# Performance work log

Measured on AMD Instinct MI355X. Metric: run time of the kernel, lower is better.

Reference implementation:

```python
import jax, jax.numpy as jnp
import numpy as np

N_EMBD = 1024
N_HEAD = 16
HEAD_DIM = N_EMBD // N_HEAD
B, T = 2, 2048


def setup_inputs() -> dict:
    key = jax.random.key(0)
    ks = jax.random.split(key, 9)
    s = 1.0 / np.sqrt(N_EMBD)
    return {
        "x": jax.random.normal(ks[0], (B, T, N_EMBD), dtype=jnp.float32),
        "Wq": jax.random.normal(ks[1], (N_EMBD, N_EMBD), dtype=jnp.float32) * s,
        "bq": jax.random.normal(ks[2], (N_EMBD,), dtype=jnp.float32) * s,
        "Wk": jax.random.normal(ks[3], (N_EMBD, N_EMBD), dtype=jnp.float32) * s,
        "bk": jax.random.normal(ks[4], (N_EMBD,), dtype=jnp.float32) * s,
        "Wv": jax.random.normal(ks[5], (N_EMBD, N_EMBD), dtype=jnp.float32) * s,
        "bv": jax.random.normal(ks[6], (N_EMBD,), dtype=jnp.float32) * s,
        "Wp": jax.random.normal(ks[7], (N_EMBD, N_EMBD), dtype=jnp.float32) * s,
        "bp": jax.random.normal(ks[8], (N_EMBD,), dtype=jnp.float32) * s,
    }


def reference(x, Wq, bq, Wk, bk, Wv, bv, Wp, bp):
    b, t, c = x.shape
    # torch Linear: y = x @ W.T + b
    def proj(W, bias):
        y = jnp.einsum('btc,oc->bto', x, W) + bias
        return y.reshape(b, t, N_HEAD, HEAD_DIM).transpose(0, 2, 1, 3)  # [B,H,T,D]

    q = proj(Wq, bq)
    k = proj(Wk, bk)
    v = proj(Wv, bv)

    scale = 1.0 / np.sqrt(HEAD_DIM).astype(np.float32)
    scores = jnp.einsum('bhqd,bhkd->bhqk', q, k) * scale  # [B,H,T,T]
    causal = jnp.tril(jnp.ones((t, t), dtype=bool))
    scores = jnp.where(causal[None, None], scores, jnp.float32(-jnp.inf))
    attn = jax.nn.softmax(scores, axis=-1)
    out = jnp.einsum('bhqk,bhkd->bhqd', attn, v)  # [B,H,T,D]
    out = out.transpose(0, 2, 1, 3).reshape(b, t, c)
    out = jnp.einsum('btc,oc->bto', out, Wp) + bp
    return out
```

## Files before the change

### kernel.cpp

```cpp
#include <hip/hip_runtime.h>
#include <hip/hip_bf16.h>

#define TT 2048
#define MM 4096

typedef __attribute__((ext_vector_type(8))) short bf16x8;
typedef __attribute__((ext_vector_type(4))) float f32x4;

__device__ inline short f2bf(float f){
  union { float f; unsigned u; } x; x.f = f;
  unsigned r = x.u + 0x7FFFu + ((x.u >> 16) & 1u);
  return (short)(r >> 16);
}
__device__ inline int pk2bf(float a, float b){
  __hip_bfloat162 h2 = __float22bfloat162_rn(make_float2(a, b));
  return *(int*)&h2;
}

__device__ inline void async16(const void* g, void* l){
  __builtin_amdgcn_global_load_lds((const __attribute__((address_space(1))) void*)g,
                                   (__attribute__((address_space(3))) void*)l, 16, 0, 0);
}

__global__ void cvt_all(const float* __restrict__ x,
                        const float* __restrict__ Wq, const float* __restrict__ Wk,
                        const float* __restrict__ Wv, const float* __restrict__ Wp,
                        short* __restrict__ xb, short* __restrict__ Wqb, short* __restrict__ Wkb,
                        short* __restrict__ Wvb, short* __restrict__ Wpb){
  int b = blockIdx.x;
  const float* in; short* out; int base;
  if (b < 4096)      { in = x;  out = xb;  base = b; }
  else if (b < 5120) { in = Wq; out = Wqb; base = b - 4096; }
  else if (b < 6144) { in = Wk; out = Wkb; base = b - 5120; }
  else if (b < 7168) { in = Wv; out = Wvb; base = b - 6144; }
  else               { in = Wp; out = Wpb; base = b - 7168; }
  int i = base * 256 + threadIdx.x;
  float4 v = ((const float4*)in)[i];
  short4 o;
  o.x = f2bf(v.x); o.y = f2bf(v.y); o.z = f2bf(v.z); o.w = f2bf(v.w);
  ((short4*)out)[i] = o;
}

__device__ inline void gemm_core(const short* __restrict__ A, const short* __restrict__ Wm,
                                 short* As, short* Bs, int m0, int n0, int k0, int nkt,
                                 int tid, int wm, int wn, int quad, int lr,
                                 f32x4 acc[4][4])
{
  const int prow = tid >> 2, pcol = (tid & 3) << 3;
  const short* Ap0 = A  + (size_t)(m0 + prow) * 1024 + k0 + pcol;
  const short* Ap1 = Ap0 + 64 * 1024;
  const short* Bp0 = Wm + (size_t)(n0 + prow) * 1024 + k0 + pcol;
  const short* Bp1 = Bp0 + 64 * 1024;
  for (int kt = 0; kt < nkt; ++kt){
    const int kk = kt * 64;
#pragma unroll
    for (int pn = 0; pn < 2; ++pn){
      async16(Ap0 + kk + pn*32, As + pn*4096 + (size_t)tid * 8);
      async16(Ap1 + kk + pn*32, As + pn*4096 + (size_t)(tid + 256) * 8);
      async16(Bp0 + kk + pn*32, Bs + pn*4096 + (size_t)tid * 8);
      async16(Bp1 + kk + pn*32, Bs + pn*4096 + (size_t)(tid + 256) * 8);
    }
    __syncthreads();
#pragma unroll
    for (int ks = 0; ks < 2; ++ks){
      bf16x8 aF[4], bF[4];
#pragma unroll
      for (int mt = 0; mt < 4; ++mt) aF[mt] = *(const bf16x8*)(As + ks*4096 + (wm*64 + mt*16 + lr)*32 + quad*8);
#pragma unroll
      for (int nt = 0; nt < 4; ++nt) bF[nt] = *(const bf16x8*)(Bs + ks*4096 + (wn*64 + nt*16 + lr)*32 + quad*8);
#pragma unroll
      for (int mt = 0; mt < 4; ++mt)
#pragma unroll
        for (int nt = 0; nt < 4; ++nt)
          acc[mt][nt] = __builtin_amdgcn_mfma_f32_16x16x32_bf16(aF[mt], bF[nt], acc[mt][nt], 0, 0, 0);
    }
    __syncthreads();
  }
}

__launch_bounds__(256, 3)
__global__ void gemm_qkv(const short* __restrict__ A,
                         const short* __restrict__ W0, const short* __restrict__ W1, const short* __restrict__ W2,
                         const float* __restrict__ b0, const float* __restrict__ b1, const float* __restrict__ b2,
                         short* __restrict__ Qo, short* __restrict__ Ko, short* __restrict__ Vt)
{
  __shared__ __align__(16) short smem[16384];
  short* As = smem;
  short* Bs = smem + 8192;
  const int bid = blockIdx.x + (blockIdx.y << 3) + (blockIdx.z << 8);
  const int xcd = bid & 7, slot = bid >> 3;
  const int z   = slot >> 5;
  const int rem = slot & 31;
  const int m0  = (((xcd << 2) + (rem >> 3))) * 128;
  const int n0  = (rem & 7) * 128;
  const short* Wm   = (z == 0) ? W0 : ((z == 1) ? W1 : W2);
  const float* bias = (z == 0) ? b0 : ((z == 1) ? b1 : b2);
  const int tid = threadIdx.x;
  const int lane = tid & 63, wave = tid >> 6;
  const int wm = wave >> 1, wn = wave & 1;
  const int quad = lane >> 4, lr = lane & 15;

  f32x4 acc[4][4];
#pragma unroll
  for (int i = 0; i < 4; ++i)
#pragma unroll
    for (int j = 0; j < 4; ++j)
#pragma unroll
      for (int r = 0; r < 4; ++r) acc[i][j][r] = 0.f;

  gemm_core(A, Wm, As, Bs, m0, n0, 0, 16, tid, wm, wn, quad, lr, acc);

  const float qscale = 0.125f * 1.4426950408889634f;
  const int bB = m0 >> 11, t0 = m0 & 2047;

  if (z == 2){
#pragma unroll
    for (int nh = 0; nh < 2; ++nh){
      __syncthreads();
      if (wn == nh){
#pragma unroll
        for (int nt = 0; nt < 4; ++nt){
          int n = n0 + wn*64 + nt*16 + lr;
          float bv = bias[n];
          int n_l = nt*16 + lr;
#pragma unroll
          for (int mt = 0; mt < 4; ++mt)
#pragma unroll
            for (int r = 0; r < 4; ++r){
              int m_l = wm*64 + mt*16 + quad*4 + r;
              smem[n_l*136 + m_l] = f2bf(acc[mt][nt][r] + bv);
            }
        }
      }
      __syncthreads();
#pragma unroll
      for (int i = 0; i < 4; ++i){
        int c = tid + i*256;
        int rowN = c >> 4, ch = c & 15;
        int4 v = *(const int4*)(smem + rowN*136 + ch*8);
        int n = n0 + nh*64 + rowN;
        int hH = n >> 6, d = n & 63;
        *(int4*)(Vt + ((size_t)((bB<<4) + hH)*64 + d)*2048 + t0 + ch*8) = v;
      }
    }
    return;
  }

  short* dst = (z == 0) ? Qo : Ko;
#pragma unroll
  for (int nh = 0; nh < 2; ++nh){
    __syncthreads();
    if (wn == nh){
#pragma unroll
      for (int nt = 0; nt < 4; ++nt){
        int n_l = nt*16 + lr;
        float bv = bias[n0 + nh*64 + n_l];
#pragma unroll
        for (int mt = 0; mt < 4; ++mt){
#pragma unroll
          for (int r = 0; r < 4; ++r){
            int m_l = wm*64 + mt*16 + quad*4 + r;
            float v = acc[mt][nt][r] + bv;
            if (z == 0) v *= qscale;
            smem[m_l*72 + n_l] = f2bf(v);
          }
        }
      }
    }
    __syncthreads();
    const int hH = (n0 + nh*64) >> 6;
    short* dhead = dst + (size_t)((bB<<4) + hH) * 2048 * 64;
#pragma unroll
    for (int i = 0; i < 4; ++i){
      int c = tid + i*256;
      int rowm = c >> 3, ch = (c & 7) << 3;
      int4 v = *(const int4*)(smem + rowm*72 + ch);
      *(int4*)(dhead + (size_t)(t0 + rowm)*64 + ch) = v;
    }
  }
}

__launch_bounds__(256, 2)
__global__ void gemm_proj(const short* __restrict__ A, const short* __restrict__ Wm,
                          const float* __restrict__ bias, float* __restrict__ out)
{
  __shared__ __align__(16) short As[2*4096];
  __shared__ __align__(16) short Bs[2*2048];
  const int bid = blockIdx.x + (blockIdx.y << 4);
  const int xcd = bid & 7, slot = bid >> 3;
  const int m0  = ((xcd << 2) + (slot >> 4)) * 128;
  const int n0  = (slot & 15) * 64;
  const int tid = threadIdx.x;
  const int lane = tid & 63, wave = tid >> 6;
  const int quad = lane >> 4, lr = lane & 15;

  const int prow = tid >> 2, pcol = (tid & 3) << 3;
  const short* Ap0 = A  + (size_t)(m0 + prow) * 1024 + pcol;
  const short* Ap1 = Ap0 + 64 * 1024;
  const short* Bp0 = Wm + (size_t)(n0 + prow) * 1024 + pcol;

  f32x4 acc[2][4];
#pragma unroll
  for (int i = 0; i < 2; ++i)
#pragma unroll
    for (int j = 0; j < 4; ++j)
#pragma unroll
      for (int r = 0; r < 4; ++r) acc[i][j][r] = 0.f;

  for (int kt = 0; kt < 16; ++kt){
    const int kk = kt * 64;
#pragma unroll
    for (int pn = 0; pn < 2; ++pn){
      async16(Ap0 + kk + pn*32, As + pn*4096 + (size_t)tid * 8);
      async16(Ap1 + kk + pn*32, As + pn*4096 + (size_t)(tid + 256) * 8);
      async16(Bp0 + kk + pn*32, Bs + pn*2048 + (size_t)tid * 8);
    }
    __syncthreads();
#pragma unroll
    for (int ks = 0; ks < 2; ++ks){
      bf16x8 aF[2], bF[4];
#pragma unroll
      for (int mt = 0; mt < 2; ++mt) aF[mt] = *(const bf16x8*)(As + ks*4096 + (wave*32 + mt*16 + lr)*32 + quad*8);
#pragma unroll
      for (int nt = 0; nt < 4; ++nt) bF[nt] = *(const bf16x8*)(Bs + ks*2048 + (nt*16 + lr)*32 + quad*8);
#pragma unroll
      for (int mt = 0; mt < 2; ++mt)
#pragma unroll
        for (int nt = 0; nt < 4; ++nt)
          acc[mt][nt] = __builtin_amdgcn_mfma_f32_16x16x32_bf16(aF[mt], bF[nt], acc[mt][nt], 0, 0, 0);
    }
    __syncthreads();
  }

#pragma unroll
  for (int nt = 0; nt < 4; ++nt){
    int n = n0 + nt*16 + lr;
    float bv = bias[n];
#pragma unroll
    for (int mt = 0; mt < 2; ++mt){
      int mBase = m0 + wave*32 + mt*16 + quad*4;
#pragma unroll
      for (int r = 0; r < 4; ++r){
        int m = mBase + r;
        out[(size_t)m * 1024 + n] = acc[mt][nt][r] + bv;
      }
    }
  }
}

__device__ __constant__ int slice_tbl[24] = {
  14352, 30736,     2,
  31760, 26638,  2052,
  12302, 27534,  4102,
  28687, 20491,  6152,
  29647, 19082, 16393,
  24589, 10252, 16969,
  25421, 21195,  8202,
  22540, 23308, 18442
};

__launch_bounds__(256, 3)
__global__ void attn_kernel(const short* __restrict__ Q, const short* __restrict__ K,
                            const short* __restrict__ Vt, short* __restrict__ AO,
                            float* __restrict__ Opart, float* __restrict__ Lpart)
{
  __shared__ __align__(16) short Ks[2][4096];
  __shared__ __align__(16) short Vs[2][4096];
  __shared__ __align__(16) short Ps[8192];
  const int tid = threadIdx.x, lane = tid & 63, wave = tid >> 6;
  const int quad = lane >> 4, lr = lane & 15;
  const int bid = blockIdx.x;
  const int a = (bid >> 5) & 7;
  const int hb = bid & 31;
  const int j = bid >> 8;
  const int e = slice_tbl[a*3 + j];
  const int qb = e >> 11, kv_s = (e >> 6) & 31, kvn = e & 63;
  const bool split = (kvn != 2*qb + 2);
  const int half = (kv_s != 0) ? 1 : 0;
  const int bidx = hb >> 4, h = hb & 15;
  const int wq0 = qb * 128 + wave * 32;
  const short* Qh = Q  + (size_t)hb * TT * 64;
  const short* Kh = K  + (size_t)hb * TT * 64;
  const short* Vh = Vt + (size_t)hb * 64 * TT;
  short* Pw = Ps + wave * 2048;

  const int srow = tid >> 3;
  const int ssw  = (tid & 7) ^ (srow & 7);
  const short* Kp0 = Kh + (size_t)srow * 64 + ssw * 8;
  const short* Vp0 = Vh + (size_t)srow * TT + ssw * 8;

  bf16x8 qf[2][2];
#pragma unroll
  for (int g = 0; g < 2; ++g)
#pragma unroll
    for (int ks = 0; ks < 2; ++ks)
      qf[g][ks] = *(const bf16x8*)(Qh + (size_t)(wq0 + g*16 + lr) * 64 + ks*32 + quad*8);

  const int lsw0 = (((0*4 + quad) ^ (lr & 7)) << 3);
  const int lsw1 = (((1*4 + quad) ^ (lr & 7)) << 3);
  const int qh2 = quad >> 1, qlo = (quad & 1) << 2;

  f32x4 acc_o[2][4], l_acc[2];
#pragma unroll
  for (int g = 0; g < 2; ++g){
#pragma unroll
    for (int r = 0; r < 4; ++r) l_acc[g][r] = 0.f;
#pragma unroll
    for (int dt = 0; dt < 4; ++dt)
#pragma unroll
      for (int r = 0; r < 4; ++r) acc_o[g][dt][r] = 0.f;
  }

  const short one_bf = (short)0x3F80;
  const bf16x8 onesf = { one_bf, one_bf, one_bf, one_bf, one_bf, one_bf, one_bf, one_bf };

  const int kv_e = kv_s + kvn;
  const int qtw = wq0 >> 6;
  {
    const short* kp = Kp0 + (size_t)kv_s * 4096;
    const short* vp = Vp0 + kv_s * 64;
    async16(kp,          &Ks[0][(size_t)tid * 8]);
    async16(kp + 32*64,  &Ks[0][(size_t)(tid + 256) * 8]);
    async16(vp,          &Vs[0][(size_t)tid * 8]);
    async16(vp + 32*TT,  &Vs[0][(size_t)(tid + 256) * 8]);
  }

  const short* kp_n = Kp0 + (size_t)(kv_s + 1) * 4096;
  const short* vp_n = Vp0 + (kv_s + 1) * 64;

  int cur = 0;
  for (int kv = kv_s; kv < kv_e; ++kv){
    const int kv0 = kv * 64;
    __syncthreads();
    if (kv + 1 < kv_e){
      const int nb = cur ^ 1;
      async16(kp_n,          &Ks[nb][(size_t)tid * 8]);
      async16(kp_n + 32*64,  &Ks[nb][(size_t)(tid + 256) * 8]);
      async16(vp_n,          &Vs[nb][(size_t)tid * 8]);
      async16(vp_n + 32*TT,  &Vs[nb][(size_t)(tid + 256) * 8]);
      kp_n += 4096; vp_n += 64;
    }
    if (kv0 <= wq0 + 31){
      __builtin_amdgcn_s_setprio(1);
      f32x4 s4[2][4];
#pragma unroll
      for (int g = 0; g < 2; ++g)
#pragma unroll
        for (int nt = 0; nt < 4; ++nt)
#pragma unroll
          for (int r = 0; r < 4; ++r) s4[g][nt][r] = 0.f;
#pragma unroll
      for (int nt = 0; nt < 4; ++nt){
        bf16x8 kf0 = *(const bf16x8*)(&Ks[cur][(nt*16 + lr)*64 + lsw0]);
        bf16x8 kf1 = *(const bf16x8*)(&Ks[cur][(nt*16 + lr)*64 + lsw1]);
#pragma unroll
        for (int g = 0; g < 2; ++g){
          s4[g][nt] = __builtin_amdgcn_mfma_f32_16x16x32_bf16(kf0, qf[g][0], s4[g][nt], 0, 0, 0);
          s4[g][nt] = __builtin_amdgcn_mfma_f32_16x16x32_bf16(kf1, qf[g][1], s4[g][nt], 0, 0, 0);
        }
      }

      if (kv == qtw){
#pragma unroll
        for (int g = 0; g < 2; ++g){
          const int qglob = wq0 + g*16 + lr;
          short* Pg = Pw + g*1024;
#pragma unroll
          for (int nt = 0; nt < 4; ++nt){
            const int keyb = kv0 + nt*16 + quad*4;
            float pv[4];
#pragma unroll
            for (int r = 0; r < 4; ++r){
              float v = exp2f(s4[g][nt][r]);
              if (keyb + r > qglob) v = 0.f;
              pv[r] = v;
            }
            int2 w;
            w.x = pk2bf(pv[0], pv[1]);
            w.y = pk2bf(pv[2], pv[3]);
            const int gg = nt*2 + qh2;
            *(int2*)(Pg + lr*64 + ((gg ^ (lr & 7)) << 3) + qlo) = w;
          }
        }
      } else {
#pragma unroll
        for (int g = 0; g < 2; ++g){
          short* Pg = Pw + g*1024;
#pragma unroll
          for (int nt = 0; nt < 4; ++nt){
            int2 w;
            w.x = pk2bf(exp2f(s4[g][nt][0]), exp2f(s4[g][nt][1]));
            w.y = pk2bf(exp2f(s4[g][nt][2]), exp2f(s4[g][nt][3]));
            const int gg = nt*2 + qh2;
            *(int2*)(Pg + lr*64 + ((gg ^ (lr & 7)) << 3) + qlo) = w;
          }
        }
      }

#pragma unroll
      for (int ks = 0; ks < 2; ++ks){
        const int lsw = ks ? lsw1 : lsw0;
        bf16x8 ptf0 = *(const bf16x8*)(Pw + lr*64 + lsw);
        bf16x8 ptf1 = *(const bf16x8*)(Pw + 1024 + lr*64 + lsw);
        l_acc[0] = __builtin_amdgcn_mfma_f32_16x16x32_bf16(onesf, ptf0, l_acc[0], 0, 0, 0);
        l_acc[1] = __builtin_amdgcn_mfma_f32_16x16x32_bf16(onesf, ptf1, l_acc[1], 0, 0, 0);
#pragma unroll
        for (int dt = 0; dt < 4; ++dt){
          bf16x8 vf = *(const bf16x8*)(&Vs[cur][(dt*16 + lr)*64 + lsw]);
          acc_o[0][dt] = __builtin_amdgcn_mfma_f32_16x16x32_bf16(vf, ptf0, acc_o[0][dt], 0, 0, 0);
          acc_o[1][dt] = __builtin_amdgcn_mfma_f32_16x16x32_bf16(vf, ptf1, acc_o[1][dt], 0, 0, 0);
        }
      }
      __builtin_amdgcn_s_setprio(0);
    }
    cur ^= 1;
  }

  if (split){
    const int p = (((hb << 3) | (qb - 8)) << 1) + half;
    float* Op = Opart + (size_t)p * 8192;
#pragma unroll
    for (int g = 0; g < 2; ++g){
      const int q_l = wave*32 + g*16 + lr;
#pragma unroll
      for (int dt = 0; dt < 4; ++dt)
        *(f32x4*)(Op + q_l*64 + dt*16 + quad*4) = acc_o[g][dt];
      if (lane < 16) Lpart[p*128 + wave*32 + g*16 + lane] = l_acc[g][0];
    }
    return;
  }

#pragma unroll
  for (int g = 0; g < 2; ++g){
    short* Pg = Pw + g*1024;
    const float inv = __builtin_amdgcn_rcpf(l_acc[g][0]);
#pragma unroll
    for (int dt = 0; dt < 4; ++dt){
      int2 w;
      w.x = pk2bf(acc_o[g][dt][0] * inv, acc_o[g][dt][1] * inv);
      w.y = pk2bf(acc_o[g][dt][2] * inv, acc_o[g][dt][3] * inv);
      const int gg = dt*2 + qh2;
      *(int2*)(Pg + lr*64 + ((gg ^ (lr & 7)) << 3) + qlo) = w;
    }
#pragma unroll
    for (int i = 0; i < 2; ++i){
      int c = lane + i*64;
      int row = c >> 3, ch = c & 7;
      int4 v = *(const int4*)(Pg + row*64 + ((ch ^ (row & 7)) << 3));
      *(int4*)(AO + (size_t)(bidx*2048 + wq0 + g*16 + row)*1024 + h*64 + ch*8) = v;
    }
  }
}

__global__ void attn_combine(const float* __restrict__ Opart, const float* __restrict__ Lpart,
                             short* __restrict__ AO)
{
  const int gid = blockIdx.x * 256 + threadIdx.x;
  const int row = gid >> 4, dq = (gid & 15) << 2;
  const int hb = row >> 10, band = (row >> 7) & 7, r = row & 127;
  const int p = ((hb << 3) | band) << 1;
  const f32x4 a = *(const f32x4*)(Opart + (size_t)p*8192 + r*64 + dq);
  const f32x4 b = *(const f32x4*)(Opart + (size_t)(p+1)*8192 + r*64 + dq);
  const float l = Lpart[p*128 + r] + Lpart[(p+1)*128 + r];
  const float inv = __builtin_amdgcn_rcpf(l);
  int2 w;
  w.x = pk2bf((a[0]+b[0])*inv, (a[1]+b[1])*inv);
  w.y = pk2bf((a[2]+b[2])*inv, (a[3]+b[3])*inv);
  const int t = (8 + band)*128 + r;
  const int bidx = hb >> 4, h = hb & 15;
  *(int2*)(AO + (size_t)(bidx*2048 + t)*1024 + h*64 + dq) = w;
}

extern "C" void kernel_launch(void* const* d_in, const int* in_sizes, int n_in,
                              void* d_out, int out_size, void* d_ws, size_t ws_size,
                              hipStream_t stream)
{
  const float* x  = (const float*)d_in[0];
  const float* Wq = (const float*)d_in[1];
  const float* bq = (const float*)d_in[2];
  const float* Wk = (const float*)d_in[3];
  const float* bk = (const float*)d_in[4];
  const float* Wv = (const float*)d_in[5];
  const float* bv = (const float*)d_in[6];
  const float* Wp = (const float*)d_in[7];
  const float* bp = (const float*)d_in[8];
  float* out = (float*)d_out;

  char* ws = (char*)d_ws;
  const size_t MB = 1024ull * 1024ull;
  short* Qb  = (short*)(ws + 0);
  short* Kb  = (short*)(ws + 8*MB);
  short* Vtb = (short*)(ws + 16*MB);
  short* AOb = (short*)(ws + 24*MB);
  short* xb  = (short*)(ws + 24*MB);
  short* Wqb = (short*)(ws + 32*MB);
  short* Wkb = (short*)(ws + 34*MB);
  short* Wvb = (short*)(ws + 36*MB);
  short* Wpb = (short*)(ws + 38*MB);
  float* Opart = (float*)(ws + 40*MB);
  float* Lpart = (float*)(ws + 56*MB);

  cvt_all<<<8192, 256, 0, stream>>>(x, Wq, Wk, Wv, Wp, xb, Wqb, Wkb, Wvb, Wpb);
  gemm_qkv<<<dim3(8, 32, 3), 256, 0, stream>>>(xb, Wqb, Wkb, Wvb, bq, bk, bv, Qb, Kb, Vtb);
  attn_kernel<<<768, 256, 0, stream>>>(Qb, Kb, Vtb, AOb, Opart, Lpart);
  attn_combine<<<2048, 256, 0, stream>>>(Opart, Lpart, AOb);
  gemm_proj<<<dim3(16, 32), 256, 0, stream>>>(AOb, Wpb, bp, out);
}
```

Measured before the change: 180.9 us.

## Double-buffer GEMM LDS tiles to overlap async loads with MFMA

Both the QKV projection and output projection GEMMs now use a two-stage ping-pong LDS buffer with 32-wide k-steps. The next tile is prefetched via global_load_lds while MFMAs run on the current tile, and there is one barrier per iteration instead of two. The aim is to hide global-load latency behind compute. The trade-off is twice as many iterations with less MFMA work per barrier. Correctness relies on the async loads finishing before the next barrier, since no explicit vmcnt wait is visible.

New measurement: 181.3 us (median of 3 runs). About the same (+0.2%).

```diff
diff --git a/kernel.cpp b/kernel.cpp
--- a/kernel.cpp
+++ b/kernel.cpp
@@ -42,39 +42,42 @@
 }
 
 __device__ inline void gemm_core(const short* __restrict__ A, const short* __restrict__ Wm,
-                                 short* As, short* Bs, int m0, int n0, int k0, int nkt,
+                                 short* As, short* Bs, int m0, int n0,
                                  int tid, int wm, int wn, int quad, int lr,
                                  f32x4 acc[4][4])
 {
   const int prow = tid >> 2, pcol = (tid & 3) << 3;
-  const short* Ap0 = A  + (size_t)(m0 + prow) * 1024 + k0 + pcol;
+  const short* Ap0 = A  + (size_t)(m0 + prow) * 1024 + pcol;
   const short* Ap1 = Ap0 + 64 * 1024;
-  const short* Bp0 = Wm + (size_t)(n0 + prow) * 1024 + k0 + pcol;
+  const short* Bp0 = Wm + (size_t)(n0 + prow) * 1024 + pcol;
   const short* Bp1 = Bp0 + 64 * 1024;
-  for (int kt = 0; kt < nkt; ++kt){
-    const int kk = kt * 64;
-#pragma unroll
-    for (int pn = 0; pn < 2; ++pn){
-      async16(Ap0 + kk + pn*32, As + pn*4096 + (size_t)tid * 8);
-      async16(Ap1 + kk + pn*32, As + pn*4096 + (size_t)(tid + 256) * 8);
-      async16(Bp0 + kk + pn*32, Bs + pn*4096 + (size_t)tid * 8);
-      async16(Bp1 + kk + pn*32, Bs + pn*4096 + (size_t)(tid + 256) * 8);
-    }
+  async16(Ap0, As + (size_t)tid * 8);
+  async16(Ap1, As + (size_t)(tid + 256) * 8);
+  async16(Bp0, Bs + (size_t)tid * 8);
+  async16(Bp1, Bs + (size_t)(tid + 256) * 8);
+  int cur = 0;
+  for (int kt = 0; kt < 32; ++kt){
     __syncthreads();
-#pragma unroll
-    for (int ks = 0; ks < 2; ++ks){
-      bf16x8 aF[4], bF[4];
-#pragma unroll
-      for (int mt = 0; mt < 4; ++mt) aF[mt] = *(const bf16x8*)(As + ks*4096 + (wm*64 + mt*16 + lr)*32 + quad*8);
-#pragma unroll
-      for (int nt = 0; nt < 4; ++nt) bF[nt] = *(const bf16x8*)(Bs + ks*4096 + (wn*64 + nt*16 + lr)*32 + quad*8);
-#pragma unroll
-      for (int mt = 0; mt < 4; ++mt)
-#pragma unroll
-        for (int nt = 0; nt < 4; ++nt)
-          acc[mt][nt] = __builtin_amdgcn_mfma_f32_16x16x32_bf16(aF[mt], bF[nt], acc[mt][nt], 0, 0, 0);
-    }
-    __syncthreads();
+    if (kt + 1 < 32){
+      const int kk = (kt + 1) * 32;
+      short* Ad = As + (cur ^ 1) * 4096;
+      short* Bd = Bs + (cur ^ 1) * 4096;
+      async16(Ap0 + kk, Ad + (size_t)tid * 8);
+      async16(Ap1 + kk, Ad + (size_t)(tid + 256) * 8);
+      async16(Bp0 + kk, Bd + (size_t)tid * 8);
+      async16(Bp1 + kk, Bd + (size_t)(tid + 256) * 8);
+    }
+    bf16x8 aF[4], bF[4];
+#pragma unroll
+    for (int mt = 0; mt < 4; ++mt) aF[mt] = *(const bf16x8*)(As + cur*4096 + (wm*64 + mt*16 + lr)*32 + quad*8);
+#pragma unroll
+    for (int nt = 0; nt < 4; ++nt) bF[nt] = *(const bf16x8*)(Bs + cur*4096 + (wn*64 + nt*16 + lr)*32 + quad*8);
+#pragma unroll
+    for (int mt = 0; mt < 4; ++mt)
+#pragma unroll
+      for (int nt = 0; nt < 4; ++nt)
+        acc[mt][nt] = __builtin_amdgcn_mfma_f32_16x16x32_bf16(aF[mt], bF[nt], acc[mt][nt], 0, 0, 0);
+    cur ^= 1;
   }
 }
 
@@ -108,7 +111,7 @@
 #pragma unroll
       for (int r = 0; r < 4; ++r) acc[i][j][r] = 0.f;
 
-  gemm_core(A, Wm, As, Bs, m0, n0, 0, 16, tid, wm, wn, quad, lr, acc);
+  gemm_core(A, Wm, As, Bs, m0, n0, tid, wm, wn, quad, lr, acc);
 
   const float qscale = 0.125f * 1.4426950408889634f;
   const int bB = m0 >> 11, t0 = m0 & 2047;
@@ -207,29 +210,31 @@
 #pragma unroll
       for (int r = 0; r < 4; ++r) acc[i][j][r] = 0.f;
 
-  for (int kt = 0; kt < 16; ++kt){
-    const int kk = kt * 64;
-#pragma unroll
-    for (int pn = 0; pn < 2; ++pn){
-      async16(Ap0 + kk + pn*32, As + pn*4096 + (size_t)tid * 8);
-      async16(Ap1 + kk + pn*32, As + pn*4096 + (size_t)(tid + 256) * 8);
-      async16(Bp0 + kk + pn*32, Bs + pn*2048 + (size_t)tid * 8);
-    }
+  async16(Ap0, As + (size_t)tid * 8);
+  async16(Ap1, As + (size_t)(tid + 256) * 8);
+  if (prow < 64) async16(Bp0, Bs + (size_t)tid * 8);
+  int cur = 0;
+  for (int kt = 0; kt < 32; ++kt){
     __syncthreads();
-#pragma unroll
-    for (int ks = 0; ks < 2; ++ks){
-      bf16x8 aF[2], bF[4];
-#pragma unroll
-      for (int mt = 0; mt < 2; ++mt) aF[mt] = *(const bf16x8*)(As + ks*4096 + (wave*32 + mt*16 + lr)*32 + quad*8);
-#pragma unroll
-      for (int nt = 0; nt < 4; ++nt) bF[nt] = *(const bf16x8*)(Bs + ks*2048 + (nt*16 + lr)*32 + quad*8);
-#pragma unroll
-      for (int mt = 0; mt < 2; ++mt)
-#pragma unroll
-        for (int nt = 0; nt < 4; ++nt)
-          acc[mt][nt] = __builtin_amdgcn_mfma_f32_16x16x32_bf16(aF[mt], bF[nt], acc[mt][nt], 0, 0, 0);
-    }
-    __syncthreads();
+    if (kt + 1 < 32){
+      const int kk = (kt + 1) * 32;
+      short* Ad = As + (cur ^ 1) * 4096;
+      short* Bd = Bs + (cur ^ 1) * 2048;
+      async16(Ap0 + kk, Ad + (size_t)tid * 8);
+      async16(Ap1 + kk, Ad + (size_t)(tid + 256) * 8);
+      if (prow < 64) async16(Bp0 + kk, Bd + (size_t)tid * 8);
+    }
+    bf16x8 aF[2], bF[4];
+#pragma unroll
+    for (int mt = 0; mt < 2; ++mt) aF[mt] = *(const bf16x8*)(As + cur*4096 + (wave*32 + mt*16 + lr)*32 + quad*8);
+#pragma unroll
+    for (int nt = 0; nt < 4; ++nt) bF[nt] = *(const bf16x8*)(Bs + cur*2048 + (nt*16 + lr)*32 + quad*8);
+#pragma unroll
+    for (int mt = 0; mt < 2; ++mt)
+#pragma unroll
+      for (int nt = 0; nt < 4; ++nt)
+        acc[mt][nt] = __builtin_amdgcn_mfma_f32_16x16x32_bf16(aF[mt], bF[nt], acc[mt][nt], 0, 0, 0);
+    cur ^= 1;
   }
 
 #pragma unroll
```
